# Optimization experiments

Hardware: AMD Instinct MI355X
Metric: run time of the kernel (lower is better)

The kernel has to match this reference:

```python
import jax, jax.numpy as jnp
import numpy as np

BN_EPS = 1e-5

def _conv1x1(x, w, b=None):
    # x: [B,C,H,W], w: [O,C] -> [B,O,H,W]
    y = jnp.einsum('bchw,oc->bohw', x, w)
    if b is not None:
        y = y + b[None, :, None, None]
    return y

def _bn_silu(y, gamma, beta):
    # BN inference with running_mean=0, running_var=1, then SiLU
    scale = gamma / jnp.sqrt(1.0 + BN_EPS)
    y = y * scale[None, :, None, None] + beta[None, :, None, None]
    return jax.nn.silu(y)

def setup_inputs() -> dict:
    key = jax.random.key(0)
    ks = jax.random.split(key, 20)
    B, D, S = 32, 512, 32
    C = D // 2
    d = {}
    d['x'] = jax.random.normal(ks[0], (B, D, S, S), jnp.float32)
    d['cv1_w'] = jax.random.normal(ks[1], (C, D), jnp.float32) * (1.0 / np.sqrt(D))
    d['cv1_gamma'] = jax.random.uniform(ks[2], (C,), jnp.float32, 0.5, 1.5)
    d['cv1_beta'] = jax.random.normal(ks[3], (C,), jnp.float32) * 0.1
    d['q_w'] = jax.random.normal(ks[4], (C, C), jnp.float32) * (1.0 / np.sqrt(C))
    d['q_b'] = jax.random.normal(ks[5], (C,), jnp.float32) * 0.02
    d['k_w'] = jax.random.normal(ks[6], (C, C), jnp.float32) * (1.0 / np.sqrt(C))
    d['k_b'] = jax.random.normal(ks[7], (C,), jnp.float32) * 0.02
    d['v_w'] = jax.random.normal(ks[8], (C, C), jnp.float32) * (1.0 / np.sqrt(C))
    d['v_b'] = jax.random.normal(ks[9], (C,), jnp.float32) * 0.02
    d['e_w'] = jax.random.normal(ks[10], (C, C), jnp.float32) * (1.0 / np.sqrt(C))
    d['e_b'] = jax.random.normal(ks[11], (C,), jnp.float32) * 0.02
    d['rel_h'] = jax.random.normal(ks[12], (1, C, S, 1), jnp.float32)
    d['rel_w'] = jax.random.normal(ks[13], (1, C, 1, S), jnp.float32)
    d['cv2_w'] = jax.random.normal(ks[14], (D, C), jnp.float32) * (1.0 / np.sqrt(C))
    d['cv2_gamma'] = jax.random.uniform(ks[15], (D,), jnp.float32, 0.5, 1.5)
    d['cv2_beta'] = jax.random.normal(ks[16], (D,), jnp.float32) * 0.1
    return d

def reference(x, cv1_w, cv1_gamma, cv1_beta, q_w, q_b, k_w, k_b, v_w, v_b,
              e_w, e_b, rel_h, rel_w, cv2_w, cv2_gamma, cv2_beta):
    # cv1: 1x1 conv (no bias) + BN + SiLU
    x1 = _bn_silu(_conv1x1(x, cv1_w), cv1_gamma, cv1_beta)  # [B,C,H,W]
    B, C, H, W = x1.shape
    N = H * W
    q = _conv1x1(x1, q_w, q_b).reshape(B, C, N)
    k = _conv1x1(x1, k_w, k_b).reshape(B, C, N)
    v = _conv1x1(x1, v_w, v_b).reshape(B, C, N)
    e = _conv1x1(x1, e_w, e_b).reshape(B, C, N)
    # content-content: q^T k -> [B,N,N]
    cc = jnp.einsum('bci,bcj->bij', q, k)
    # content-position: (rel_h + rel_w) flattened to [C,N], times extra proj
    pos = (rel_h + rel_w).reshape(C, N)  # broadcast add -> [1,C,H,W] -> [C,N]
    cp = jnp.einsum('ci,bcj->bij', pos, e)  # [B,N,N]
    attn = jax.nn.softmax(cc + cp, axis=-1)
    # out[b,c,i] = sum_j v[b,c,j] * attn[b,i,j]
    out = jnp.einsum('bcj,bij->bci', v, attn).reshape(B, C, H, W)
    y = _bn_silu(_conv1x1(out, cv2_w), cv2_gamma, cv2_beta)
    return x + y
```

## Files before the change

kernel.cpp:

```cpp
#include <hip/hip_runtime.h>
#include <hip/hip_bf16.h>

typedef unsigned short u16;
typedef __attribute__((ext_vector_type(8))) _Float16 half8;
typedef __attribute__((ext_vector_type(4))) float f32x4;

__device__ __forceinline__ u16 f2h(float f) {
  _Float16 h = (_Float16)f;
  union { _Float16 h; u16 u; } a; a.h = h;
  return a.u;
}

__device__ __forceinline__ float h2f(u16 u) {
  union { _Float16 h; u16 u; } a; a.u = u;
  return (float)a.h;
}

__device__ __forceinline__ float silu_f(float y) {
  return y / (1.0f + __expf(-y));
}

__device__ __forceinline__ void glds16(const u16* g, u16* l) {
  __builtin_amdgcn_global_load_lds(
      (__attribute__((address_space(1))) unsigned*)(g),
      (__attribute__((address_space(3))) unsigned*)(l), 16, 0, 0);
}

enum { EPI_BNSILU_N = 0, EPI_QKEV, EPI_RAW_F16, EPI_BNSILU_RES_M };

template<int EPI, bool DUAL, int TILES, int GX>
__global__ __launch_bounds__(256, 2)
void gemm_nt(const u16* __restrict__ A, long long a_bs, int lda,
             const u16* __restrict__ A2,
             const u16* __restrict__ B, long long b_bs, int ldb,
             void* __restrict__ C0, long long c_bs, int ldc,
             void* __restrict__ C1, void* __restrict__ C2,
             int K,
             const float* __restrict__ p0, const float* __restrict__ p1,
             const float* __restrict__ res, long long res_bs)
{
  __shared__ u16 smem[32768];

  const int id = blockIdx.x;
  const int bz = (id & 7) + 8 * (id / (8 * TILES));
  const int tt = (id >> 3) % TILES;
  const int bm = tt % GX;
  const int bn = tt / GX;
  const u16* Ab = A + (long long)bz * a_bs;
  const u16* Bb = B + (long long)bz * b_bs;
  const int m0 = bm * 128;
  const int n0 = bn * 128;
  const int t = threadIdx.x;
  const int lane = t & 63;
  const int w = t >> 6;
  const int wm = (w & 1) * 64;
  const int wn = (w >> 1) * 64;
  const int q = lane >> 4;
  const int lr = lane & 15;

  f32x4 acc[4][4];
#pragma unroll
  for (int i = 0; i < 4; ++i)
#pragma unroll
    for (int j = 0; j < 4; ++j)
      acc[i][j] = (f32x4){0.f, 0.f, 0.f, 0.f};

  const int lrow = lane >> 2;
  const int kch = (lane & 3) ^ ((lane >> 2) & 3) ^ ((lane >> 4) & 3);
  const int lk = kch * 8;
  const u16* aR0 = Ab + (long long)(m0 + 32 * w + lrow) * lda + lk;
  const u16* aR1 = aR0 + 16LL * lda;
  const u16* bR0 = Bb + (long long)(n0 + 32 * w + lrow) * ldb + lk;
  const u16* bR1 = bR0 + 16LL * ldb;
  const u16* a2R0 = nullptr; const u16* a2R1 = nullptr;
  if constexpr (DUAL) {
    a2R0 = A2 + (long long)(m0 + 32 * w + lrow) * 256 + lk;
    a2R1 = a2R0 + 16LL * 256;
  }
  u16* la0 = smem + w * 1024;         u16* la1 = la0 + 512;
  u16* lb0 = smem + 16384 + w * 1024; u16* lb1 = lb0 + 512;
  const int fpos = (q ^ (lr & 3) ^ ((lr >> 2) & 3)) * 8;

  for (int k0 = 0; k0 < K; k0 += 128) {
    __syncthreads();
    if (!DUAL || k0 < 256) {
#pragma unroll
      for (int s = 0; s < 4; ++s) {
        const int ko = k0 + 32 * s;
        glds16(aR0 + ko, la0 + s * 4096);
        glds16(aR1 + ko, la1 + s * 4096);
      }
    } else {
#pragma unroll
      for (int s = 0; s < 4; ++s) {
        const int ko = k0 - 256 + 32 * s;
        glds16(a2R0 + ko, la0 + s * 4096);
        glds16(a2R1 + ko, la1 + s * 4096);
      }
    }
#pragma unroll
    for (int s = 0; s < 4; ++s) {
      const int ko = k0 + 32 * s;
      glds16(bR0 + ko, lb0 + s * 4096);
      glds16(bR1 + ko, lb1 + s * 4096);
    }
    __syncthreads();
#pragma unroll
    for (int h = 0; h < 4; ++h) {
      half8 af[4], bfr[4];
#pragma unroll
      for (int i = 0; i < 4; ++i)
        af[i] = *(const half8*)&smem[h * 4096 + (wm + i * 16 + lr) * 32 + fpos];
#pragma unroll
      for (int j = 0; j < 4; ++j)
        bfr[j] = *(const half8*)&smem[16384 + h * 4096 + (wn + j * 16 + lr) * 32 + fpos];
#pragma unroll
      for (int i = 0; i < 4; ++i)
#pragma unroll
        for (int j = 0; j < 4; ++j)
          acc[i][j] = __builtin_amdgcn_mfma_f32_16x16x32_f16(af[i], bfr[j], acc[i][j], 0, 0, 0);
    }
  }

  if constexpr (EPI == EPI_BNSILU_N) {
    u16* Cg = (u16*)C0 + (long long)bz * c_bs;
#pragma unroll
    for (int i = 0; i < 4; ++i)
#pragma unroll
      for (int j = 0; j < 4; ++j)
#pragma unroll
        for (int r = 0; r < 4; ++r) {
          const int m = m0 + wm + i * 16 + q * 4 + r;
          const int n = n0 + wn + j * 16 + lr;
          float v = acc[i][j][r];
          v = silu_f(v * (p0[n] * 0.99999500003749969f) + p1[n]);
          Cg[(long long)m * ldc + n] = f2h(v);
        }
  } else if constexpr (EPI == EPI_RAW_F16) {
    u16* Cg = (u16*)C0 + (long long)bz * c_bs;
#pragma unroll
    for (int i = 0; i < 4; ++i)
#pragma unroll
      for (int j = 0; j < 4; ++j)
#pragma unroll
        for (int r = 0; r < 4; ++r) {
          const int m = m0 + wm + i * 16 + q * 4 + r;
          const int n = n0 + wn + j * 16 + lr;
          Cg[(long long)m * ldc + n] = f2h(acc[i][j][r]);
        }
  } else if constexpr (EPI == EPI_BNSILU_RES_M) {
    float* Cg = (float*)C0 + (long long)bz * c_bs;
    const float* rg = res + (long long)bz * res_bs;
#pragma unroll
    for (int i = 0; i < 4; ++i)
#pragma unroll
      for (int j = 0; j < 4; ++j)
#pragma unroll
        for (int r = 0; r < 4; ++r) {
          const int m = m0 + wm + i * 16 + q * 4 + r;
          const int n = n0 + wn + j * 16 + lr;
          float v = acc[i][j][r];
          v = silu_f(v * (p0[m] * 0.99999500003749969f) + p1[m]);
          const long long idx = (long long)m * ldc + n;
          Cg[idx] = v + rg[idx];
        }
  } else {
    const int seg = n0 >> 8;
    const int nb = n0 & 255;
    if (seg < 3) {
      u16* dst; long long bs; int ld2;
      if (seg == 0) { dst = (u16*)C0; bs = 262144; ld2 = 256; }
      else { dst = (u16*)C1 + (seg == 2 ? 256 : 0); bs = 524288; ld2 = 512; }
      dst += (long long)bz * bs;
#pragma unroll
      for (int i = 0; i < 4; ++i)
#pragma unroll
        for (int j = 0; j < 4; ++j)
#pragma unroll
          for (int r = 0; r < 4; ++r) {
            const int m = m0 + wm + i * 16 + q * 4 + r;
            const int col = wn + j * 16 + lr;
            float v = acc[i][j][r] + p0[n0 + col];
            dst[(long long)m * ld2 + nb + col] = f2h(v);
          }
    } else {
      u16* dst = (u16*)C2 + (long long)bz * 262144;
#pragma unroll
      for (int s = 0; s < 4; ++s) {
        const int rbase = s * 32;
        __syncthreads();
        if (wm == (rbase & 64)) {
          const int ibase = (rbase & 32) >> 4;
#pragma unroll
          for (int ii = 0; ii < 2; ++ii) {
            const int i = ibase + ii;
#pragma unroll
            for (int j = 0; j < 4; ++j)
#pragma unroll
              for (int r = 0; r < 4; ++r) {
                const int row32 = i * 16 + q * 4 + r - (rbase & 32);
                const int col = wn + j * 16 + lr;
                float v = acc[i][j][r] + p0[768 + nb + col];
                smem[row32 * 132 + col] = f2h(v);
              }
          }
        }
        __syncthreads();
#pragma unroll
        for (int p = 0; p < 2; ++p) {
          const int lin = p * 256 + t;
          const int c = lin >> 2;
          const int mc = lin & 3;
          u16 tmp[8];
#pragma unroll
          for (int r8 = 0; r8 < 8; ++r8)
            tmp[r8] = smem[(mc * 8 + r8) * 132 + c];
          *(half8*)&dst[(long long)(nb + c) * 1024 + m0 + rbase + mc * 8] =
              *(const half8*)tmp;
        }
      }
    }
  }
}

template<bool DUAL>
__global__ __launch_bounds__(512, 2)
void gemm256_nt(const u16* __restrict__ A, long long a_bs, int lda,
                const u16* __restrict__ A2,
                const u16* __restrict__ B, long long b_bs, int ldb,
                u16* __restrict__ C0, long long c_bs, int ldc, int K)
{
  __shared__ u16 smem[32768];

  const int id = blockIdx.x;
  const int bz = (id & 7) + 8 * (id / (8 * 16));
  const int tt = (id >> 3) % 16;
  const int m0 = (tt & 3) * 256;
  const int n0 = (tt >> 2) * 256;
  const u16* Ab = A + (long long)bz * a_bs;
  const u16* Bb = B + (long long)bz * b_bs;
  const int t = threadIdx.x;
  const int lane = t & 63;
  const int w = t >> 6;
  const int wm = (w & 1) * 128;
  const int wn = (w >> 1) * 64;
  const int q = lane >> 4;
  const int lr = lane & 15;

  f32x4 acc[8][4];
#pragma unroll
  for (int i = 0; i < 8; ++i)
#pragma unroll
    for (int j = 0; j < 4; ++j)
      acc[i][j] = (f32x4){0.f, 0.f, 0.f, 0.f};

  const int lrow = lane >> 2;
  const int kch = (lane & 3) ^ ((lane >> 2) & 3) ^ ((lane >> 4) & 3);
  const int lk = kch * 8;
  const u16* aR0 = Ab + (long long)(m0 + 32 * w + lrow) * lda + lk;
  const u16* aR1 = aR0 + 16LL * lda;
  const u16* bR0 = Bb + (long long)(n0 + 32 * w + lrow) * ldb + lk;
  const u16* bR1 = bR0 + 16LL * ldb;
  const u16* a2R0 = nullptr; const u16* a2R1 = nullptr;
  if constexpr (DUAL) {
    a2R0 = A2 + (long long)(m0 + 32 * w + lrow) * 256 + lk;
    a2R1 = a2R0 + 16LL * 256;
  }
  u16* la0 = smem + w * 1024;         u16* la1 = la0 + 512;
  u16* lb0 = smem + 16384 + w * 1024; u16* lb1 = lb0 + 512;
  const int fpos = (q ^ (lr & 3) ^ ((lr >> 2) & 3)) * 8;

  for (int k0 = 0; k0 < K; k0 += 64) {
    __syncthreads();
    if (!DUAL || k0 < 256) {
      glds16(aR0 + k0, la0);        glds16(aR1 + k0, la1);
      glds16(aR0 + k0 + 32, la0 + 8192); glds16(aR1 + k0 + 32, la1 + 8192);
    } else {
      glds16(a2R0 + (k0 - 256), la0);        glds16(a2R1 + (k0 - 256), la1);
      glds16(a2R0 + (k0 - 224), la0 + 8192); glds16(a2R1 + (k0 - 224), la1 + 8192);
    }
    glds16(bR0 + k0, lb0);        glds16(bR1 + k0, lb1);
    glds16(bR0 + k0 + 32, lb0 + 8192); glds16(bR1 + k0 + 32, lb1 + 8192);
    __syncthreads();
#pragma unroll
    for (int h = 0; h < 2; ++h) {
      half8 bfr[4];
#pragma unroll
      for (int j = 0; j < 4; ++j)
        bfr[j] = *(const half8*)&smem[16384 + h * 8192 + (wn + j * 16 + lr) * 32 + fpos];
#pragma unroll
      for (int i = 0; i < 8; ++i) {
        const half8 af = *(const half8*)&smem[h * 8192 + (wm + i * 16 + lr) * 32 + fpos];
#pragma unroll
        for (int j = 0; j < 4; ++j)
          acc[i][j] = __builtin_amdgcn_mfma_f32_16x16x32_f16(af, bfr[j], acc[i][j], 0, 0, 0);
      }
    }
  }

  u16* Cg = C0 + (long long)bz * c_bs;
#pragma unroll
  for (int i = 0; i < 8; ++i)
#pragma unroll
    for (int j = 0; j < 4; ++j)
#pragma unroll
      for (int r = 0; r < 4; ++r) {
        const int m = m0 + wm + i * 16 + q * 4 + r;
        const int n = n0 + wn + j * 16 + lr;
        Cg[(long long)m * ldc + n] = f2h(acc[i][j][r]);
      }
}

__global__ __launch_bounds__(256)
void transpose_x(const float* __restrict__ x, u16* __restrict__ xT) {
  __shared__ float tile[64][65];
  const int b = blockIdx.z;
  const int n0 = blockIdx.x * 64;
  const int d0 = blockIdx.y * 64;
  const int t = threadIdx.x;
  const float* src = x + (long long)b * 524288;
  const int rr = t >> 4;
  const int cc = t & 15;
#pragma unroll
  for (int i = 0; i < 4; ++i) {
    const int r = rr + i * 16;
    const float4 v = *(const float4*)&src[(long long)(d0 + r) * 1024 + n0 + cc * 4];
    tile[r][cc * 4 + 0] = v.x;
    tile[r][cc * 4 + 1] = v.y;
    tile[r][cc * 4 + 2] = v.z;
    tile[r][cc * 4 + 3] = v.w;
  }
  __syncthreads();
  u16* dst = xT + (long long)b * 524288;
  const int d8 = t & 7;
  const int nn = t >> 3;
#pragma unroll
  for (int i = 0; i < 2; ++i) {
    const int n = nn + i * 32;
    u16 tmp[8];
#pragma unroll
    for (int e = 0; e < 8; ++e) tmp[e] = f2h(tile[d8 * 8 + e][n]);
    *(half8*)&dst[(long long)(n0 + n) * 512 + d0 + d8 * 8] = *(const half8*)tmp;
  }
}

__global__ __launch_bounds__(256)
void convert_w(const float* __restrict__ w1, const float* __restrict__ wq,
               const float* __restrict__ wk, const float* __restrict__ wv,
               const float* __restrict__ we, const float* __restrict__ w2,
               const float* __restrict__ bq, const float* __restrict__ bk,
               const float* __restrict__ be, const float* __restrict__ bv,
               u16* __restrict__ dstw, float* __restrict__ bbuf) {
  int id = blockIdx.x * 256 + threadIdx.x;
  if (id < 524288) {
    float v;
    if (id < 131072) v = w1[id];
    else if (id < 393216) {
      int s = id - 131072, o = s >> 8, c = s & 255;
      if (o < 256) v = wq[o * 256 + c];
      else if (o < 512) v = wk[(o - 256) * 256 + c];
      else if (o < 768) v = we[(o - 512) * 256 + c];
      else v = wv[(o - 768) * 256 + c];
    } else v = w2[id - 393216];
    dstw[id] = f2h(v);
  } else {
    int i = id - 524288;
    float v;
    if (i < 256) v = bq[i];
    else if (i < 512) v = bk[i - 256];
    else if (i < 768) v = be[i - 512];
    else v = bv[i - 768];
    bbuf[i] = v;
  }
}

__global__ __launch_bounds__(256)
void pos_compute(const float* __restrict__ rh, const float* __restrict__ rw,
                 u16* __restrict__ posT) {
  const int n = blockIdx.x;
  const int c = threadIdx.x;
  posT[n * 256 + c] = f2h(rh[c * 32 + (n >> 5)] + rw[c * 32 + (n & 31)]);
}

__global__ __launch_bounds__(256)
void softmax_rows(u16* __restrict__ logits) {
  __shared__ float redm[2][2], reds[2][2];
  const int t = threadIdx.x;
  const int row = t >> 7;
  const int l = t & 127;
  const int wv = (t >> 6) & 1;
  u16* p = logits + (long long)blockIdx.x * 2048 + row * 1024;
  half8 raw = ((const half8*)p)[l];
  float v[8];
#pragma unroll
  for (int e = 0; e < 8; ++e) v[e] = (float)raw[e];
  float mx = v[0];
#pragma unroll
  for (int e = 1; e < 8; ++e) mx = fmaxf(mx, v[e]);
#pragma unroll
  for (int off = 32; off > 0; off >>= 1) mx = fmaxf(mx, __shfl_down(mx, off));
  if ((t & 63) == 0) redm[row][wv] = mx;
  __syncthreads();
  mx = fmaxf(redm[row][0], redm[row][1]);
  float ev[8];
  float s = 0.f;
#pragma unroll
  for (int e = 0; e < 8; ++e) { ev[e] = __expf(v[e] - mx); s += ev[e]; }
#pragma unroll
  for (int off = 32; off > 0; off >>= 1) s += __shfl_down(s, off);
  if ((t & 63) == 0) reds[row][wv] = s;
  __syncthreads();
  const float inv = 1.0f / (reds[row][0] + reds[row][1]);
  half8 o;
#pragma unroll
  for (int e = 0; e < 8; ++e) o[e] = (_Float16)(ev[e] * inv);
  ((half8*)p)[l] = o;
}

extern "C" void kernel_launch(void* const* d_in, const int* in_sizes, int n_in,
                              void* d_out, int out_size, void* d_ws, size_t ws_size,
                              hipStream_t stream) {
  const float* x  = (const float*)d_in[0];
  const float* w1 = (const float*)d_in[1];
  const float* g1 = (const float*)d_in[2];
  const float* b1 = (const float*)d_in[3];
  const float* wq = (const float*)d_in[4];
  const float* bq = (const float*)d_in[5];
  const float* wk = (const float*)d_in[6];
  const float* bk = (const float*)d_in[7];
  const float* wv = (const float*)d_in[8];
  const float* bv = (const float*)d_in[9];
  const float* we = (const float*)d_in[10];
  const float* be = (const float*)d_in[11];
  const float* rh = (const float*)d_in[12];
  const float* rw = (const float*)d_in[13];
  const float* w2 = (const float*)d_in[14];
  const float* g2 = (const float*)d_in[15];
  const float* b2 = (const float*)d_in[16];
  float* out = (float*)d_out;
  char* ws = (char*)d_ws;

  u16* xT     = (u16*)(ws + 0);
  u16* x1t    = (u16*)(ws + 33554432);
  u16* qbuf   = (u16*)(ws + 50331648);
  u16* kcat   = (u16*)(ws + 67108864);
  u16* vbuf   = (u16*)(ws + 100663296);
  u16* outt   = (u16*)(ws + 117440512);
  u16* posT   = (u16*)(ws + 134217728);
  u16* wbuf   = (u16*)(ws + 134742016);
  float* bbuf = (float*)(ws + 135790592);
  u16* logits = (u16*)(ws + 142606336);

  u16* w1b    = wbuf;
  u16* wqkve  = wbuf + 131072;
  u16* w2b    = wbuf + 393216;

  transpose_x<<<dim3(16, 8, 32), 256, 0, stream>>>(x, xT);
  convert_w<<<dim3(2052), 256, 0, stream>>>(w1, wq, wk, wv, we, w2,
                                            bq, bk, be, bv, wbuf, bbuf);
  pos_compute<<<dim3(1024), 256, 0, stream>>>(rh, rw, posT);

  gemm_nt<EPI_BNSILU_N, false, 16, 8><<<dim3(512), 256, 0, stream>>>(
      xT, 524288LL, 512, nullptr, w1b, 0LL, 512,
      x1t, 262144LL, 256, nullptr, nullptr, 512, g1, b1, nullptr, 0LL);

  gemm_nt<EPI_QKEV, false, 64, 8><<<dim3(2048), 256, 0, stream>>>(
      x1t, 262144LL, 256, nullptr, wqkve, 0LL, 256,
      qbuf, 262144LL, 256, kcat, vbuf, 256, bbuf, nullptr, nullptr, 0LL);

  gemm256_nt<true><<<dim3(512), 512, 0, stream>>>(
      qbuf, 262144LL, 256, posT, kcat, 524288LL, 512,
      logits, 1048576LL, 1024, 512);

  softmax_rows<<<dim3(16384), 256, 0, stream>>>(logits);

  gemm_nt<EPI_RAW_F16, false, 16, 8><<<dim3(512), 256, 0, stream>>>(
      logits, 1048576LL, 1024, nullptr, vbuf, 262144LL, 1024,
      outt, 262144LL, 256, nullptr, nullptr, 1024, nullptr, nullptr, nullptr, 0LL);

  gemm_nt<EPI_BNSILU_RES_M, false, 32, 4><<<dim3(1024), 256, 0, stream>>>(
      w2b, 0LL, 256, nullptr, outt, 262144LL, 256,
      out, 524288LL, 1024, nullptr, nullptr, 256, g2, b2, x, 524288LL);
}
```

Baseline: 327.1 us.

## Software-pipeline GEMM K-loop with two LDS half-stages and vmcnt waits

```diff
diff --git a/kernel.cpp b/kernel.cpp
--- a/kernel.cpp
+++ b/kernel.cpp
@@ -266,37 +266,57 @@
     a2R0 = A2 + (long long)(m0 + 32 * w + lrow) * 256 + lk;
     a2R1 = a2R0 + 16LL * 256;
   }
-  u16* la0 = smem + w * 1024;         u16* la1 = la0 + 512;
-  u16* lb0 = smem + 16384 + w * 1024; u16* lb1 = lb0 + 512;
   const int fpos = (q ^ (lr & 3) ^ ((lr >> 2) & 3)) * 8;
 
+#define STAGE256(kk, p)                                                       \
+  do {                                                                        \
+    u16* _a = smem + (p) * 8192 + w * 1024;                                   \
+    u16* _b = smem + 16384 + (p) * 8192 + w * 1024;                           \
+    if (!DUAL || (kk) < 256) {                                                \
+      glds16(aR0 + (kk), _a);  glds16(aR1 + (kk), _a + 512);                  \
+    } else {                                                                  \
+      glds16(a2R0 + ((kk) - 256), _a);  glds16(a2R1 + ((kk) - 256), _a + 512);\
+    }                                                                         \
+    glds16(bR0 + (kk), _b);  glds16(bR1 + (kk), _b + 512);                    \
+  } while (0)
+
+#define COMPUTE256(p)                                                         \
+  do {                                                                        \
+    half8 bfr[4];                                                             \
+    _Pragma("unroll")                                                         \
+    for (int j = 0; j < 4; ++j)                                               \
+      bfr[j] = *(const half8*)&smem[16384 + (p) * 8192 + (wn + j * 16 + lr) * 32 + fpos]; \
+    _Pragma("unroll")                                                         \
+    for (int i = 0; i < 8; ++i) {                                             \
+      const half8 af = *(const half8*)&smem[(p) * 8192 + (wm + i * 16 + lr) * 32 + fpos]; \
+      _Pragma("unroll")                                                       \
+      for (int j = 0; j < 4; ++j)                                             \
+        acc[i][j] = __builtin_amdgcn_mfma_f32_16x16x32_f16(af, bfr[j], acc[i][j], 0, 0, 0); \
+    }                                                                         \
+  } while (0)
+
+  STAGE256(0, 0);
+  STAGE256(32, 1);
   for (int k0 = 0; k0 < K; k0 += 64) {
-    __syncthreads();
-    if (!DUAL || k0 < 256) {
-      glds16(aR0 + k0, la0);        glds16(aR1 + k0, la1);
-      glds16(aR0 + k0 + 32, la0 + 8192); glds16(aR1 + k0 + 32, la1 + 8192);
+    asm volatile("s_waitcnt vmcnt(4)" ::: "memory");
+    __builtin_amdgcn_s_barrier();
+    COMPUTE256(0);
+    __builtin_amdgcn_sched_barrier(0);
+    __builtin_amdgcn_s_barrier();
+    if (k0 + 64 < K) {
+      STAGE256(k0 + 64, 0);
+      asm volatile("s_waitcnt vmcnt(4)" ::: "memory");
     } else {
-      glds16(a2R0 + (k0 - 256), la0);        glds16(a2R1 + (k0 - 256), la1);
-      glds16(a2R0 + (k0 - 224), la0 + 8192); glds16(a2R1 + (k0 - 224), la1 + 8192);
+      asm volatile("s_waitcnt vmcnt(0)" ::: "memory");
     }
-    glds16(bR0 + k0, lb0);        glds16(bR1 + k0, lb1);
-    glds16(bR0 + k0 + 32, lb0 + 8192); glds16(bR1 + k0 + 32, lb1 + 8192);
-    __syncthreads();
-#pragma unroll
-    for (int h = 0; h < 2; ++h) {
-      half8 bfr[4];
-#pragma unroll
-      for (int j = 0; j < 4; ++j)
-        bfr[j] = *(const half8*)&smem[16384 + h * 8192 + (wn + j * 16 + lr) * 32 + fpos];
-#pragma unroll
-      for (int i = 0; i < 8; ++i) {
-        const half8 af = *(const half8*)&smem[h * 8192 + (wm + i * 16 + lr) * 32 + fpos];
-#pragma unroll
-        for (int j = 0; j < 4; ++j)
-          acc[i][j] = __builtin_amdgcn_mfma_f32_16x16x32_f16(af, bfr[j], acc[i][j], 0, 0, 0);
-      }
-    }
-  }
+    __builtin_amdgcn_s_barrier();
+    COMPUTE256(1);
+    __builtin_amdgcn_sched_barrier(0);
+    __builtin_amdgcn_s_barrier();
+    if (k0 + 96 < K) STAGE256(k0 + 96, 1);
+  }
+#undef STAGE256
+#undef COMPUTE256
 
   u16* Cg = C0 + (long long)bz * c_bs;
 #pragma unroll
```

Result: faster. 319.9 us (-2.2%).
